# Performance work log

Measured on AMD Instinct MI355X. Metric: run time of the kernel, lower is better.

Reference implementation:

```python
import jax, jax.numpy as jnp
import numpy as np

B, T = 512, 64
C_IN, C_HID, C_OUT = 512, 512, 256
SIZE_INP = C_IN + C_HID + C_OUT  # 1280
SIZE_GATES = 4 * C_HID           # 2048


def setup_inputs() -> dict:
    key = jax.random.key(0)
    k1, k2, k3, k4, k5 = jax.random.split(key, 5)
    s_rnn = 1.0 / np.sqrt(SIZE_INP)
    s_feat = 1.0 / np.sqrt(C_HID)
    return {
        "z": jax.random.normal(k1, (B, T, C_IN, 1, 1), dtype=jnp.float32),
        "r0": jnp.zeros((B, C_OUT, 1, 1), dtype=jnp.float32),
        "h0": jnp.zeros((B, C_HID, 1, 1), dtype=jnp.float32),
        "c0": jnp.zeros((B, C_HID, 1, 1), dtype=jnp.float32),
        "W_rnn": jax.random.uniform(k2, (SIZE_GATES, SIZE_INP), jnp.float32, -s_rnn, s_rnn),
        "b_rnn": jax.random.uniform(k3, (SIZE_GATES,), jnp.float32, -s_rnn, s_rnn),
        "W_feat": jax.random.uniform(k4, (C_OUT, C_HID), jnp.float32, -s_feat, s_feat),
        "b_feat": jax.random.uniform(k5, (C_OUT,), jnp.float32, -s_feat, s_feat),
    }


def reference(z, r0, h0, c0, W_rnn, b_rnn, W_feat, b_feat):
    # 1x1 convs on [B,C,1,1] tensors are plain matmuls over channels.
    zs = z[..., 0, 0]  # [B, T, C_in]

    def step(carry, z_t):
        r, h, c = carry  # [B,Cout], [B,H], [B,H]
        inp = jnp.concatenate([r, h, z_t], axis=1)          # [B, 1280]
        gates = inp @ W_rnn.T + b_rnn                       # [B, 4H]
        f, i, s, o = jnp.split(gates, 4, axis=1)            # torch.chunk order
        c_n = jax.nn.sigmoid(f) * c + jax.nn.sigmoid(i) * jnp.tanh(s)
        h_n = jax.nn.sigmoid(o) * jnp.tanh(c_n)
        r_n = r + h_n @ W_feat.T + b_feat
        return (r_n, h_n, c_n), None

    carry0 = (r0[..., 0, 0], h0[..., 0, 0], c0[..., 0, 0])
    (r, h, c), _ = jax.lax.scan(step, carry0, jnp.swapaxes(zs, 0, 1))
    return r[..., None, None], (h[..., None, None], c[..., None, None])
```

## Files before the change

kernel.cpp:

```cpp
#include <hip/hip_runtime.h>
#include <hip/hip_fp16.h>


using f32x4 = __attribute__((ext_vector_type(4))) float;
using f16x8 = __attribute__((ext_vector_type(8))) _Float16;
using fp16x2 = __attribute__((ext_vector_type(2))) __fp16;

union U4H8 { uint4 u; f16x8 h; fp16x2 p[4]; };

__device__ __forceinline__ float sigm(float x){ return 1.0f/(1.0f + __expf(-x)); }
__device__ __forceinline__ float tanhfast(float x){
  x = fminf(fmaxf(x, -30.f), 30.f);
  float e = __expf(2.0f*x);
  return (e - 1.0f)/(e + 1.0f);
}

#define MFMA16(a,b,c) __builtin_amdgcn_mfma_f32_16x16x32_f16((a).h,(b).h,(c),0,0,0)


__global__ void k_wft(const float* __restrict__ wf, float* __restrict__ wft){
  int idx = blockIdx.x*256 + threadIdx.x;
  int c = idx & 511; int j = idx >> 9;
  wft[c*256 + j] = wf[idx];
}

__global__ void k_bias2(const float* __restrict__ wrnn, const float* __restrict__ brnn,
                        const float* __restrict__ bfeat, float* __restrict__ biasp){
  int wv = (blockIdx.x*256 + threadIdx.x) >> 6;
  int lane = threadIdx.x & 63;
  int g = (wv&3)*512 + (wv>>2);
  const float* wr = wrnn + (size_t)g*1280;
  float s = 0.f;
  for (int j = lane; j < 256; j += 64) s += bfeat[j]*wr[j];
  for (int off = 32; off; off >>= 1) s += __shfl_down(s, off, 64);
  if (lane == 0) biasp[wv] = brnn[g] + s;
}

__global__ void k_whp4(const float* __restrict__ wrnn, const float* __restrict__ wft,
                       float* __restrict__ whp_part){
  int s = blockIdx.x >> 8;
  int tl = blockIdx.x & 255;
  int bn = tl & 31, bk = tl >> 5;
  __shared__ float wrs[64][37];
  __shared__ float wfs[64][37];
  int tid = threadIdx.x;
  int tn = tid & 15, tk = tid >> 4;
  float accv[4][4];
  #pragma unroll
  for (int x=0;x<4;x++) for (int y=0;y<4;y++) accv[x][y]=0.f;
  for (int jc = s*64; jc < s*64+64; jc += 32){
    __syncthreads();
    for (int idx = tid; idx < 64*32; idx += 256){
      int r = idx >> 5, j = idx & 31;
      int n = bn*64 + r; int g = (n&3)*512 + (n>>2);
      wrs[r][j] = wrnn[(size_t)g*1280 + jc + j];
      wfs[r][j] = wft[(bk*64 + r)*256 + jc + j];
    }
    __syncthreads();
    for (int j=0;j<32;j++){
      float a[4], b[4];
      #pragma unroll
      for (int x=0;x<4;x++){ a[x] = wfs[tk*4+x][j]; b[x] = wrs[tn*4+x][j]; }
      #pragma unroll
      for (int x=0;x<4;x++)
        #pragma unroll
        for (int y=0;y<4;y++) accv[x][y] += a[x]*b[y];
    }
  }
  float* dst = whp_part + (size_t)s*1048576;
  for (int x=0;x<4;x++){
    int kk = bk*64 + tk*4 + x;
    for (int y=0;y<4;y++){
      int n = bn*64 + tn*4 + y;
      dst[(size_t)kk*2048 + n] = accv[x][y];
    }
  }
}

__global__ void k_whpadd(const float* __restrict__ p, float* __restrict__ o){
  int i = (blockIdx.x*256 + threadIdx.x)*4;
  float4 a = *(const float4*)(p + i);
  float4 b = *(const float4*)(p + 1048576 + i);
  float4 c = *(const float4*)(p + 2097152 + i);
  float4 d = *(const float4*)(p + 3145728 + i);
  float4 r;
  r.x = a.x+b.x+c.x+d.x; r.y = a.y+b.y+c.y+d.y;
  r.z = a.z+b.z+c.z+d.z; r.w = a.w+b.w+c.w+d.w;
  *(float4*)(o + i) = r;
}

__global__ void k_rinit(const float* __restrict__ r0, const float* __restrict__ h0,
                        const float* __restrict__ wft, const float* __restrict__ bfeat,
                        float* __restrict__ rd32, __half* __restrict__ rd16){
  __shared__ float hs[512];
  int row = blockIdx.x; int j = threadIdx.x;
  for (int k = threadIdx.x; k < 512; k += 256) hs[k] = h0[row*512 + k];
  __syncthreads();
  float acc = 0.f;
  for (int k=0;k<512;k++) acc += hs[k]*wft[k*256 + j];
  float rr = r0[row*256 + j] - acc - bfeat[j];
  rd32[row*256 + j] = rr;
  int ridx = (((row>>4)*8 + (j>>5))*64 + (row&15) + (((j&31)>>3)<<4))*8 + (j&7);
  rd16[ridx] = __float2half(rr);
}

__global__ void k_packh0(const float* __restrict__ h0, const float* __restrict__ c0,
                         __half* __restrict__ h16, float* __restrict__ c32){
  int idx = blockIdx.x*256 + threadIdx.x;
  int e = idx & 7, l = (idx>>3) & 63, kc = (idx>>9) & 15, mt = idx >> 13;
  int row = mt*16 + (l&15);
  int k = kc*32 + ((l>>4)<<3) + e;
  h16[idx] = __float2half(h0[row*512 + k]);
  c32[idx] = c0[idx];
}

__global__ void k_pack(const float* __restrict__ wrnn, const float* __restrict__ whp32,
                       const float* __restrict__ wfeat, __half* __restrict__ dst,
                       int mode, int NT16, int KCH){
  int tot = NT16*KCH*512;
  for (int idx = blockIdx.x*256 + threadIdx.x; idx < tot; idx += gridDim.x*256){
    int e = idx & 7; int l = (idx>>3) & 63;
    int kc = (idx>>9) % KCH; int nt = (idx>>9) / KCH;
    int k = kc*32 + ((l>>4)<<3) + e;
    int n = nt*16 + (l&15);
    float v;
    if (mode == 0){
      int g = (n&3)*512 + (n>>2);
      if (k < 256) v = wrnn[(size_t)g*1280 + k];
      else         v = whp32[(size_t)(k-256)*2048 + n] + wrnn[(size_t)g*1280 + k];
    } else if (mode == 2){
      int g = (n&3)*512 + (n>>2);
      v = wrnn[(size_t)g*1280 + 768 + k];
    } else {
      v = wfeat[(size_t)n*512 + k];
    }
    dst[idx] = __float2half(v);
  }
}

__global__ void k_zpackall(const float* __restrict__ z, __half* __restrict__ z16){
  int u = blockIdx.x*256 + threadIdx.x;
  int k0 = (u & 63) * 8;
  int b4 = (u >> 6) & 127;
  int t  = u >> 13;
  int b = b4 * 4;
  int frag = (t*32 + (b>>4))*16 + (k0>>5);
  uint4 wv[4];
  #pragma unroll
  for (int j=0;j<4;j++){
    const float4* src = (const float4*)(z + ((size_t)((b+j)*64 + t))*512 + k0);
    float4 f0 = src[0], f1 = src[1];
    U4H8 a;
    a.p[0] = __builtin_amdgcn_cvt_pkrtz(f0.x, f0.y);
    a.p[1] = __builtin_amdgcn_cvt_pkrtz(f0.z, f0.w);
    a.p[2] = __builtin_amdgcn_cvt_pkrtz(f1.x, f1.y);
    a.p[3] = __builtin_amdgcn_cvt_pkrtz(f1.z, f1.w);
    wv[j] = a.u;
  }
  uint4* dst = (uint4*)z16 + (size_t)frag*64 + (b & 15) + (((k0 & 31) >> 3) << 4);
  #pragma unroll
  for (int j=0;j<4;j++) dst[j] = wv[j];
}

__global__ __launch_bounds__(512) void k_gzbig(const __half* __restrict__ z16,
    const __half* __restrict__ bpz, const float* __restrict__ biasp,
    __half* __restrict__ gz){
  const int tid = threadIdx.x, lane = tid & 63, w = tid >> 6;
  const int wr = w >> 2, wc = w & 3;
  const int xcd = blockIdx.x & 7;
  const int bn  = (blockIdx.x >> 3) & 15;
  const int bmh = blockIdx.x >> 7;
  const int bm  = xcd*32 + bmh;
  const int tt = bm >> 2, bq = bm & 3;
  const int mt0 = tt*32 + bq*8 + wr*4;
  const int nt0 = bn*8 + wc*2;
  const uint4* A = (const uint4*)z16 + (size_t)(mt0*16)*64 + lane;
  const uint4* B = (const uint4*)bpz + (size_t)(nt0*16)*64 + lane;
  f32x4 acc[4][2];
  #pragma unroll
  for (int mi=0;mi<4;mi++){ acc[mi][0]=(f32x4){0,0,0,0}; acc[mi][1]=(f32x4){0,0,0,0}; }
  #pragma unroll 4
  for (int kc=0; kc<16; ++kc){
    U4H8 b0v, b1v;
    b0v.u = B[kc*64];
    b1v.u = B[(16+kc)*64];
    #pragma unroll
    for (int mi=0; mi<4; mi++){
      U4H8 a;
      a.u = A[(mi*16 + kc)*64];
      acc[mi][0] = MFMA16(a, b0v, acc[mi][0]);
      acc[mi][1] = MFMA16(a, b1v, acc[mi][1]);
    }
  }
  #pragma unroll
  for (int ns=0; ns<2; ns++){
    int n = (nt0 + ns)*16 + (lane & 15);
    float bp = biasp[n];
    #pragma unroll
    for (int mi=0; mi<4; mi++){
      #pragma unroll
      for (int i=0; i<4; i++){
        int brow = bq*128 + wr*64 + mi*16 + ((lane>>4)<<2) + i;
        gz[((size_t)(tt*512 + brow))*2048 + n] = __float2half(acc[mi][ns][i] + bp);
      }
    }
  }
}

__global__ __launch_bounds__(640) void k_stepF(
    const __half* __restrict__ rd16_in, const __half* __restrict__ h16_in,
    float* __restrict__ rd32,
    __half* __restrict__ rd16_out, __half* __restrict__ h16_out,
    float* __restrict__ c32,
    const __half* __restrict__ gz,
    const __half* __restrict__ bp_rec, const __half* __restrict__ bf_pack,
    const float* __restrict__ bfeat,
    float* __restrict__ out_h, float* __restrict__ out_c, float* __restrict__ out_r,
    int step, int mode){
  __shared__ float cls[64][69];
  const int tid = threadIdx.x, lane = tid & 63;
  const int bid = blockIdx.x;
  const int bm = (bid>>3) & 7;
  const int bn = (bid&7)*4 + (bid>>6);

  if (tid < 512){
    if (mode == 0){
      const int w = tid >> 6, wr = w >> 2, wc = w & 3;
      f32x4 a0A=(f32x4){0,0,0,0}, a0B=(f32x4){0,0,0,0};
      f32x4 a1A=(f32x4){0,0,0,0}, a1B=(f32x4){0,0,0,0};
      const int mtA = bm*4 + wr*2;
      const int nt  = bn*4 + wc;
      const uint4* a0p = (const uint4*)rd16_in + (size_t)(mtA*8)*64 + lane;
      const uint4* a1p = a0p + 8*64;
      const uint4* h0p = (const uint4*)h16_in + (size_t)(mtA*16)*64 + lane;
      const uint4* h1p = h0p + 16*64;
      const uint4* bp  = (const uint4*)bp_rec + (size_t)(nt*24)*64 + lane;
      #pragma unroll
      for (int kc=0; kc<4; ++kc){
        U4H8 a0,a1,b;
        a0.u = a0p[kc*64]; a1.u = a1p[kc*64]; b.u = bp[kc*64];
        a0A = MFMA16(a0,b,a0A);
        a1A = MFMA16(a1,b,a1A);
      }
      #pragma unroll
      for (int kc=4; kc<8; ++kc){
        U4H8 a0,a1,b;
        a0.u = a0p[kc*64]; a1.u = a1p[kc*64]; b.u = bp[kc*64];
        a0B = MFMA16(a0,b,a0B);
        a1B = MFMA16(a1,b,a1B);
      }
      #pragma unroll 4
      for (int kc=0; kc<8; ++kc){
        U4H8 a0,a1,b;
        a0.u = h0p[kc*64]; a1.u = h1p[kc*64]; b.u = bp[(8+kc)*64];
        a0A = MFMA16(a0,b,a0A);
        a1A = MFMA16(a1,b,a1A);
      }
      #pragma unroll 4
      for (int kc=8; kc<16; ++kc){
        U4H8 a0,a1,b;
        a0.u = h0p[kc*64]; a1.u = h1p[kc*64]; b.u = bp[(8+kc)*64];
        a0B = MFMA16(a0,b,a0B);
        a1B = MFMA16(a1,b,a1B);
      }
      const f32x4 acc0 = a0A + a0B;
      const f32x4 acc1 = a1A + a1B;
      #pragma unroll
      for (int i=0; i<4; i++){
        cls[wr*32 +      ((lane>>4)<<2) + i][wc*16 + (lane&15)] = acc0[i];
        cls[wr*32 + 16 + ((lane>>4)<<2) + i][wc*16 + (lane&15)] = acc1[i];
      }
    }
  } else {
    const int w2 = (tid - 512) >> 6;
    const int rb = bid*2 + w2;
    const int mt = rb >> 4;
    const int nc = rb & 15;
    const uint4* hp = (const uint4*)h16_in + (size_t)(mt*16)*64 + lane;
    const uint4* bf = (const uint4*)bf_pack + (size_t)(nc*16)*64 + lane;
    f32x4 r0v = (f32x4){0,0,0,0}, r1v = (f32x4){0,0,0,0};
    #pragma unroll 4
    for (int kc=0; kc<8; ++kc){
      U4H8 a,b;
      a.u = hp[kc*64]; b.u = bf[kc*64];
      r0v = MFMA16(a,b,r0v);
    }
    #pragma unroll 4
    for (int kc=8; kc<16; ++kc){
      U4H8 a,b;
      a.u = hp[kc*64]; b.u = bf[kc*64];
      r1v = MFMA16(a,b,r1v);
    }
    const f32x4 racc = r0v + r1v;
    const int col = nc*16 + (lane&15);
    const float bfv = bfeat[col];
    #pragma unroll
    for (int i=0;i<4;i++){
      const int grow = mt*16 + ((lane>>4)<<2) + i;
      const size_t x = (size_t)grow*256 + col;
      const float rr = racc[i] + rd32[x] + bfv;
      if (mode == 1){
        out_r[x] = rr;
      } else {
        rd32[x] = rr;
        const int ridx = (((grow>>4)*8 + (col>>5))*64
                          + (grow&15) + (((col&31)>>3)<<4))*8 + (col&7);
        rd16_out[ridx] = __float2half(rr);
      }
    }
  }

  if (mode == 0){
    __syncthreads();
    if (tid < 512){
      const __half* gzt = gz + (size_t)step*1048576;
      #pragma unroll
      for (int rep=0; rep<2; rep++){
        int idx = rep*512 + tid;
        int jl = idx & 15, row = idx >> 4;
        int grow = bm*64 + row;
        int j = bn*16 + jl;
        const __half2* gp = (const __half2*)(gzt + (size_t)grow*2048 + bn*64 + jl*4);
        __half2 p0 = gp[0], p1 = gp[1];
        float g0 = cls[row][jl*4+0] + __half2float(p0.x);
        float g1 = cls[row][jl*4+1] + __half2float(p0.y);
        float g2 = cls[row][jl*4+2] + __half2float(p1.x);
        float g3 = cls[row][jl*4+3] + __half2float(p1.y);
        float cold = c32[(size_t)grow*512 + j];
        float f  = sigm(g0);
        float ii = sigm(g1);
        float s  = tanhfast(g2);
        float o  = sigm(g3);
        float cn = f*cold + ii*s;
        float hn = o*tanhfast(cn);
        c32[(size_t)grow*512 + j] = cn;
        int hidx = (((grow>>4)*16 + (j>>5))*64 + (grow&15) + (((j&31)>>3)<<4))*8 + (j&7);
        h16_out[hidx] = __float2half(hn);
        if (step == 63){
          out_h[(size_t)grow*512 + j] = hn;
          out_c[(size_t)grow*512 + j] = cn;
        }
      }
    }
  }
}

extern "C" void kernel_launch(void* const* d_in, const int* in_sizes, int n_in,
                              void* d_out, int out_size, void* d_ws, size_t ws_size,
                              hipStream_t stream){
  const float* z     = (const float*)d_in[0];
  const float* r0    = (const float*)d_in[1];
  const float* h0    = (const float*)d_in[2];
  const float* c0    = (const float*)d_in[3];
  const float* wrnn  = (const float*)d_in[4];
  const float* brnn  = (const float*)d_in[5];
  const float* wfeat = (const float*)d_in[6];
  const float* bfeat = (const float*)d_in[7];
  float* out = (float*)d_out;

  char* wsb = (char*)d_ws;
  size_t off = 0;
  auto alloc = [&](size_t bytes)->char*{
    char* p = wsb + off; off = (off + bytes + 255) & ~(size_t)255; return p;
  };
  __half* z16     = (__half*)alloc((size_t)64*512*512*2);
  __half* bp_rec  = (__half*)alloc((size_t)128*24*512*2);
  __half* bpz     = (__half*)alloc((size_t)128*16*512*2);
  __half* bf_pack = (__half*)alloc((size_t)16*16*512*2);
  float*  biasp   = (float*) alloc(2048*4);
  float*  wft32   = (float*) alloc((size_t)512*256*4);
  __half* h16A    = (__half*)alloc((size_t)512*512*2);
  __half* h16B    = (__half*)alloc((size_t)512*512*2);
  __half* rd16A   = (__half*)alloc((size_t)512*256*2);
  __half* rd16B   = (__half*)alloc((size_t)512*256*2);
  float*  rd32    = (float*) alloc((size_t)512*256*4);
  float*  c32     = (float*) alloc((size_t)512*512*4);
  __half* gz      = (__half*)alloc((size_t)64*512*2048*2);
  (void)ws_size;
  float* whp32    = (float*)gz;
  float* whp_part = (float*)gz + 1048576;

  k_wft     <<<dim3(512),  dim3(256), 0, stream>>>(wfeat, wft32);
  k_bias2   <<<dim3(512),  dim3(256), 0, stream>>>(wrnn, brnn, bfeat, biasp);
  k_whp4    <<<dim3(1024), dim3(256), 0, stream>>>(wrnn, wft32, whp_part);
  k_whpadd  <<<dim3(1024), dim3(256), 0, stream>>>(whp_part, whp32);
  k_rinit   <<<dim3(512),  dim3(256), 0, stream>>>(r0, h0, wft32, bfeat, rd32, rd16A);
  k_packh0  <<<dim3(1024), dim3(256), 0, stream>>>(h0, c0, h16A, c32);
  k_pack    <<<dim3(1024), dim3(256), 0, stream>>>(wrnn, whp32, wfeat, bp_rec, 0, 128, 24);
  k_pack    <<<dim3(1024), dim3(256), 0, stream>>>(wrnn, whp32, wfeat, bpz,    2, 128, 16);
  k_pack    <<<dim3(64),   dim3(256), 0, stream>>>(wrnn, whp32, wfeat, bf_pack,3,  16, 16);
  k_zpackall<<<dim3(2048), dim3(256), 0, stream>>>(z, z16);
  k_gzbig   <<<dim3(4096), dim3(512), 0, stream>>>(z16, bpz, biasp, gz);

  __half* h16in = h16A;  __half* h16out = h16B;
  __half* rd16in = rd16A; __half* rd16out = rd16B;
  for (int t = 1; t <= 64; ++t){
    k_stepF<<<dim3(256), dim3(640), 0, stream>>>(
        rd16in, h16in, rd32, rd16out, h16out, c32, gz,
        bp_rec, bf_pack, bfeat,
        out + 131072, out + 393216, (float*)nullptr, t-1, 0);
    __half* th;
    th = h16in; h16in = h16out; h16out = th;
    th = rd16in; rd16in = rd16out; rd16out = th;
  }
  k_stepF<<<dim3(256), dim3(640), 0, stream>>>(
      rd16in, h16in, rd32, rd16out, h16out, c32, gz,
      bp_rec, bf_pack, bfeat,
      (float*)nullptr, (float*)nullptr, out, 64, 1);
}
```

Before: 808.7 us.

## Merge preprocessing kernels and prefetch gate/state loads in recurrent step

Folds the many setup kernels (weight transpose, bias, partial-sum reduction, packing, z conversion) into two multi-role launches, so fewer launches are issued and the whp partial sums are reduced inline during packing. Inside the per-step kernel, the precomputed z-gate values and old cell state are loaded before the MFMA loop, and the r-update warps load rd32 early, to hide global latency. The r-update branch now runs in parallel with the gate branch instead of before a shared barrier. The gz GEMM unroll drops from 4 to 2. The merged kernels use heterogeneous block roles, and the early loads raise register pressure.

Measured after the change: 752.1 us, median of 2. 7.0% less time.

```diff
diff --git a/kernel.cpp b/kernel.cpp
--- a/kernel.cpp
+++ b/kernel.cpp
@@ -7,6 +7,7 @@
 using fp16x2 = __attribute__((ext_vector_type(2))) __fp16;
 
 union U4H8 { uint4 u; f16x8 h; fp16x2 p[4]; };
+union GZU { uint2 u; __half2 h2[2]; };
 
 __device__ __forceinline__ float sigm(float x){ return 1.0f/(1.0f + __expf(-x)); }
 __device__ __forceinline__ float tanhfast(float x){
@@ -17,23 +18,24 @@
 
 #define MFMA16(a,b,c) __builtin_amdgcn_mfma_f32_16x16x32_f16((a).h,(b).h,(c),0,0,0)
 
-
-__global__ void k_wft(const float* __restrict__ wf, float* __restrict__ wft){
-  int idx = blockIdx.x*256 + threadIdx.x;
-  int c = idx & 511; int j = idx >> 9;
-  wft[c*256 + j] = wf[idx];
-}
-
-__global__ void k_bias2(const float* __restrict__ wrnn, const float* __restrict__ brnn,
-                        const float* __restrict__ bfeat, float* __restrict__ biasp){
-  int wv = (blockIdx.x*256 + threadIdx.x) >> 6;
-  int lane = threadIdx.x & 63;
-  int g = (wv&3)*512 + (wv>>2);
-  const float* wr = wrnn + (size_t)g*1280;
-  float s = 0.f;
-  for (int j = lane; j < 256; j += 64) s += bfeat[j]*wr[j];
-  for (int off = 32; off; off >>= 1) s += __shfl_down(s, off, 64);
-  if (lane == 0) biasp[wv] = brnn[g] + s;
+__global__ void k_init(const float* __restrict__ wfeat, const float* __restrict__ wrnn,
+                       const float* __restrict__ brnn, const float* __restrict__ bfeat,
+                       float* __restrict__ wft, float* __restrict__ biasp){
+  const int bid = blockIdx.x, tid = threadIdx.x;
+  if (bid < 512){
+    int idx = bid*256 + tid;
+    int c = idx & 511; int j = idx >> 9;
+    wft[c*256 + j] = wfeat[idx];
+  } else {
+    int wv = ((bid-512)*256 + tid) >> 6;
+    int lane = tid & 63;
+    int g = (wv&3)*512 + (wv>>2);
+    const float* wr = wrnn + (size_t)g*1280;
+    float s = 0.f;
+    for (int j = lane; j < 256; j += 64) s += bfeat[j]*wr[j];
+    for (int off = 32; off; off >>= 1) s += __shfl_down(s, off, 64);
+    if (lane == 0) biasp[wv] = brnn[g] + s;
+  }
 }
 
 __global__ void k_whp4(const float* __restrict__ wrnn, const float* __restrict__ wft,
@@ -77,89 +79,94 @@
   }
 }
 
-__global__ void k_whpadd(const float* __restrict__ p, float* __restrict__ o){
-  int i = (blockIdx.x*256 + threadIdx.x)*4;
-  float4 a = *(const float4*)(p + i);
-  float4 b = *(const float4*)(p + 1048576 + i);
-  float4 c = *(const float4*)(p + 2097152 + i);
-  float4 d = *(const float4*)(p + 3145728 + i);
-  float4 r;
-  r.x = a.x+b.x+c.x+d.x; r.y = a.y+b.y+c.y+d.y;
-  r.z = a.z+b.z+c.z+d.z; r.w = a.w+b.w+c.w+d.w;
-  *(float4*)(o + i) = r;
-}
-
-__global__ void k_rinit(const float* __restrict__ r0, const float* __restrict__ h0,
-                        const float* __restrict__ wft, const float* __restrict__ bfeat,
-                        float* __restrict__ rd32, __half* __restrict__ rd16){
+__global__ void k_prep(const float* __restrict__ z,
+                       const float* __restrict__ r0, const float* __restrict__ h0,
+                       const float* __restrict__ c0,
+                       const float* __restrict__ wrnn, const float* __restrict__ wfeat,
+                       const float* __restrict__ wft, const float* __restrict__ bfeat,
+                       const float* __restrict__ whp_part,
+                       float* __restrict__ rd32, __half* __restrict__ rd16,
+                       __half* __restrict__ h16, float* __restrict__ c32,
+                       __half* __restrict__ bp_rec, __half* __restrict__ bpz,
+                       __half* __restrict__ bf_pack, __half* __restrict__ z16){
   __shared__ float hs[512];
-  int row = blockIdx.x; int j = threadIdx.x;
-  for (int k = threadIdx.x; k < 512; k += 256) hs[k] = h0[row*512 + k];
-  __syncthreads();
-  float acc = 0.f;
-  for (int k=0;k<512;k++) acc += hs[k]*wft[k*256 + j];
-  float rr = r0[row*256 + j] - acc - bfeat[j];
-  rd32[row*256 + j] = rr;
-  int ridx = (((row>>4)*8 + (j>>5))*64 + (row&15) + (((j&31)>>3)<<4))*8 + (j&7);
-  rd16[ridx] = __float2half(rr);
-}
-
-__global__ void k_packh0(const float* __restrict__ h0, const float* __restrict__ c0,
-                         __half* __restrict__ h16, float* __restrict__ c32){
-  int idx = blockIdx.x*256 + threadIdx.x;
-  int e = idx & 7, l = (idx>>3) & 63, kc = (idx>>9) & 15, mt = idx >> 13;
-  int row = mt*16 + (l&15);
-  int k = kc*32 + ((l>>4)<<3) + e;
-  h16[idx] = __float2half(h0[row*512 + k]);
-  c32[idx] = c0[idx];
-}
-
-__global__ void k_pack(const float* __restrict__ wrnn, const float* __restrict__ whp32,
-                       const float* __restrict__ wfeat, __half* __restrict__ dst,
-                       int mode, int NT16, int KCH){
-  int tot = NT16*KCH*512;
-  for (int idx = blockIdx.x*256 + threadIdx.x; idx < tot; idx += gridDim.x*256){
-    int e = idx & 7; int l = (idx>>3) & 63;
-    int kc = (idx>>9) % KCH; int nt = (idx>>9) / KCH;
+  const int bid = blockIdx.x, tid = threadIdx.x;
+  if (bid < 512){
+    const int row = bid, j = tid;
+    for (int k = tid; k < 512; k += 256) hs[k] = h0[row*512 + k];
+    __syncthreads();
+    float acc = 0.f;
+    for (int k=0;k<512;k++) acc += hs[k]*wft[k*256 + j];
+    float rr = r0[row*256 + j] - acc - bfeat[j];
+    rd32[row*256 + j] = rr;
+    int ridx = (((row>>4)*8 + (j>>5))*64 + (row&15) + (((j&31)>>3)<<4))*8 + (j&7);
+    rd16[ridx] = __float2half(rr);
+  } else if (bid < 1536){
+    int idx = (bid-512)*256 + tid;
+    int e = idx & 7, l = (idx>>3) & 63, kc = (idx>>9) & 15, mt = idx >> 13;
+    int row = mt*16 + (l&15);
     int k = kc*32 + ((l>>4)<<3) + e;
-    int n = nt*16 + (l&15);
-    float v;
-    if (mode == 0){
+    h16[idx] = __float2half(h0[row*512 + k]);
+    c32[idx] = c0[idx];
+  } else if (bid < 2560){
+    const int tot = 128*24*512;
+    for (int idx = (bid-1536)*256 + tid; idx < tot; idx += 1024*256){
+      int e = idx & 7; int l = (idx>>3) & 63;
+      int kc = (idx>>9) % 24; int nt = (idx>>9) / 24;
+      int k = kc*32 + ((l>>4)<<3) + e;
+      int n = nt*16 + (l&15);
       int g = (n&3)*512 + (n>>2);
+      float v;
       if (k < 256) v = wrnn[(size_t)g*1280 + k];
-      else         v = whp32[(size_t)(k-256)*2048 + n] + wrnn[(size_t)g*1280 + k];
-    } else if (mode == 2){
+      else {
+        size_t o = (size_t)(k-256)*2048 + n;
+        v = whp_part[o] + whp_part[1048576+o] + whp_part[2097152+o]
+            + whp_part[3145728+o] + wrnn[(size_t)g*1280 + k];
+      }
+      bp_rec[idx] = __float2half(v);
+    }
+  } else if (bid < 3072){
+    const int tot = 128*16*512;
+    for (int idx = (bid-2560)*256 + tid; idx < tot; idx += 512*256){
+      int e = idx & 7; int l = (idx>>3) & 63;
+      int kc = (idx>>9) & 15; int nt = (idx>>9) >> 4;
+      int k = kc*32 + ((l>>4)<<3) + e;
+      int n = nt*16 + (l&15);
       int g = (n&3)*512 + (n>>2);
-      v = wrnn[(size_t)g*1280 + 768 + k];
-    } else {
-      v = wfeat[(size_t)n*512 + k];
-    }
-    dst[idx] = __float2half(v);
-  }
-}
-
-__global__ void k_zpackall(const float* __restrict__ z, __half* __restrict__ z16){
-  int u = blockIdx.x*256 + threadIdx.x;
-  int k0 = (u & 63) * 8;
-  int b4 = (u >> 6) & 127;
-  int t  = u >> 13;
-  int b = b4 * 4;
-  int frag = (t*32 + (b>>4))*16 + (k0>>5);
-  uint4 wv[4];
-  #pragma unroll
-  for (int j=0;j<4;j++){
-    const float4* src = (const float4*)(z + ((size_t)((b+j)*64 + t))*512 + k0);
-    float4 f0 = src[0], f1 = src[1];
-    U4H8 a;
-    a.p[0] = __builtin_amdgcn_cvt_pkrtz(f0.x, f0.y);
-    a.p[1] = __builtin_amdgcn_cvt_pkrtz(f0.z, f0.w);
-    a.p[2] = __builtin_amdgcn_cvt_pkrtz(f1.x, f1.y);
-    a.p[3] = __builtin_amdgcn_cvt_pkrtz(f1.z, f1.w);
-    wv[j] = a.u;
-  }
-  uint4* dst = (uint4*)z16 + (size_t)frag*64 + (b & 15) + (((k0 & 31) >> 3) << 4);
-  #pragma unroll
-  for (int j=0;j<4;j++) dst[j] = wv[j];
+      bpz[idx] = __float2half(wrnn[(size_t)g*1280 + 768 + k]);
+    }
+  } else if (bid < 3136){
+    const int tot = 16*16*512;
+    for (int idx = (bid-3072)*256 + tid; idx < tot; idx += 64*256){
+      int e = idx & 7; int l = (idx>>3) & 63;
+      int kc = (idx>>9) & 15; int nt = (idx>>9) >> 4;
+      int k = kc*32 + ((l>>4)<<3) + e;
+      int n = nt*16 + (l&15);
+      bf_pack[idx] = __float2half(wfeat[(size_t)n*512 + k]);
+    }
+  } else {
+    int u = (bid-3136)*256 + tid;
+    int k0 = (u & 63) * 8;
+    int b4 = (u >> 6) & 127;
+    int t  = u >> 13;
+    int b = b4 * 4;
+    int frag = (t*32 + (b>>4))*16 + (k0>>5);
+    uint4 wv[4];
+    #pragma unroll
+    for (int j=0;j<4;j++){
+      const float4* src = (const float4*)(z + ((size_t)((b+j)*64 + t))*512 + k0);
+      float4 f0 = src[0], f1 = src[1];
+      U4H8 a;
+      a.p[0] = __builtin_amdgcn_cvt_pkrtz(f0.x, f0.y);
+      a.p[1] = __builtin_amdgcn_cvt_pkrtz(f0.z, f0.w);
+      a.p[2] = __builtin_amdgcn_cvt_pkrtz(f1.x, f1.y);
+      a.p[3] = __builtin_amdgcn_cvt_pkrtz(f1.z, f1.w);
+      wv[j] = a.u;
+    }
+    uint4* dst = (uint4*)z16 + (size_t)frag*64 + (b & 15) + (((k0 & 31) >> 3) << 4);
+    #pragma unroll
+    for (int j=0;j<4;j++) dst[j] = wv[j];
+  }
 }
 
 __global__ __launch_bounds__(512) void k_gzbig(const __half* __restrict__ z16,
@@ -179,7 +186,7 @@
   f32x4 acc[4][2];
   #pragma unroll
   for (int mi=0;mi<4;mi++){ acc[mi][0]=(f32x4){0,0,0,0}; acc[mi][1]=(f32x4){0,0,0,0}; }
-  #pragma unroll 4
+  #pragma unroll 2
   for (int kc=0; kc<16; ++kc){
     U4H8 b0v, b1v;
     b0v.u = B[kc*64];
@@ -225,6 +232,17 @@
 
   if (tid < 512){
     if (mode == 0){
+      const __half* gzt = gz + (size_t)step*1048576;
+      const int jl0 = tid & 15,        row0 = tid >> 4;
+      const int jl1 = (512+tid) & 15,  row1 = (512+tid) >> 4;
+      const int gr0 = bm*64 + row0, j0 = bn*16 + jl0;
+      const int gr1 = bm*64 + row1, j1 = bn*16 + jl1;
+      GZU gu0, gu1;
+      gu0.u = *(const uint2*)(gzt + (size_t)gr0*2048 + bn*64 + jl0*4);
+      gu1.u = *(const uint2*)(gzt + (size_t)gr1*2048 + bn*64 + jl1*4);
+      const float cold0 = c32[(size_t)gr0*512 + j0];
+      const float cold1 = c32[(size_t)gr1*512 + j1];
+
       const int w = tid >> 6, wr = w >> 2, wc = w & 3;
       f32x4 a0A=(f32x4){0,0,0,0}, a0B=(f32x4){0,0,0,0};
       f32x4 a1A=(f32x4){0,0,0,0}, a1B=(f32x4){0,0,0,0};
@@ -270,63 +288,19 @@
         cls[wr*32 +      ((lane>>4)<<2) + i][wc*16 + (lane&15)] = acc0[i];
         cls[wr*32 + 16 + ((lane>>4)<<2) + i][wc*16 + (lane&15)] = acc1[i];
       }
-    }
-  } else {
-    const int w2 = (tid - 512) >> 6;
-    const int rb = bid*2 + w2;
-    const int mt = rb >> 4;
-    const int nc = rb & 15;
-    const uint4* hp = (const uint4*)h16_in + (size_t)(mt*16)*64 + lane;
-    const uint4* bf = (const uint4*)bf_pack + (size_t)(nc*16)*64 + lane;
-    f32x4 r0v = (f32x4){0,0,0,0}, r1v = (f32x4){0,0,0,0};
-    #pragma unroll 4
-    for (int kc=0; kc<8; ++kc){
-      U4H8 a,b;
-      a.u = hp[kc*64]; b.u = bf[kc*64];
-      r0v = MFMA16(a,b,r0v);
-    }
-    #pragma unroll 4
-    for (int kc=8; kc<16; ++kc){
-      U4H8 a,b;
-      a.u = hp[kc*64]; b.u = bf[kc*64];
-      r1v = MFMA16(a,b,r1v);
-    }
-    const f32x4 racc = r0v + r1v;
-    const int col = nc*16 + (lane&15);
-    const float bfv = bfeat[col];
-    #pragma unroll
-    for (int i=0;i<4;i++){
-      const int grow = mt*16 + ((lane>>4)<<2) + i;
-      const size_t x = (size_t)grow*256 + col;
-      const float rr = racc[i] + rd32[x] + bfv;
-      if (mode == 1){
-        out_r[x] = rr;
-      } else {
-        rd32[x] = rr;
-        const int ridx = (((grow>>4)*8 + (col>>5))*64
-                          + (grow&15) + (((col&31)>>3)<<4))*8 + (col&7);
-        rd16_out[ridx] = __float2half(rr);
-      }
-    }
-  }
-
-  if (mode == 0){
-    __syncthreads();
-    if (tid < 512){
-      const __half* gzt = gz + (size_t)step*1048576;
+      __syncthreads();
       #pragma unroll
       for (int rep=0; rep<2; rep++){
-        int idx = rep*512 + tid;
-        int jl = idx & 15, row = idx >> 4;
-        int grow = bm*64 + row;
-        int j = bn*16 + jl;
-        const __half2* gp = (const __half2*)(gzt + (size_t)grow*2048 + bn*64 + jl*4);
-        __half2 p0 = gp[0], p1 = gp[1];
-        float g0 = cls[row][jl*4+0] + __half2float(p0.x);
-        float g1 = cls[row][jl*4+1] + __half2float(p0.y);
-        float g2 = cls[row][jl*4+2] + __half2float(p1.x);
-        float g3 = cls[row][jl*4+3] + __half2float(p1.y);
-        float cold = c32[(size_t)grow*512 + j];
+        const int row = rep ? row1 : row0;
+        const int jl  = rep ? jl1  : jl0;
+        const int grow = rep ? gr1 : gr0;
+        const int j   = rep ? j1 : j0;
+        const GZU gu  = rep ? gu1 : gu0;
+        const float cold = rep ? cold1 : cold0;
+        float g0 = cls[row][jl*4+0] + __half2float(gu.h2[0].x);
+        float g1 = cls[row][jl*4+1] + __half2float(gu.h2[0].y);
+        float g2 = cls[row][jl*4+2] + __half2float(gu.h2[1].x);
+        float g3 = cls[row][jl*4+3] + __half2float(gu.h2[1].y);
         float f  = sigm(g0);
         float ii = sigm(g1);
         float s  = tanhfast(g2);
@@ -340,6 +314,49 @@
           out_h[(size_t)grow*512 + j] = hn;
           out_c[(size_t)grow*512 + j] = cn;
         }
+      }
+    }
+  } else {
+    const int w2 = (tid - 512) >> 6;
+    const int rb = bid*2 + w2;
+    const int mt = rb >> 4;
+    const int nc = rb & 15;
+    const int col = nc*16 + (lane&15);
+    float rdp[4];
+    #pragma unroll
+    for (int i=0;i<4;i++){
+      const int grow = mt*16 + ((lane>>4)<<2) + i;
+      rdp[i] = rd32[(size_t)grow*256 + col];
+    }
+    const float bfv = bfeat[col];
+    const uint4* hp = (const uint4*)h16_in + (size_t)(mt*16)*64 + lane;
+    const uint4* bf = (const uint4*)bf_pack + (size_t)(nc*16)*64 + lane;
+    f32x4 r0v = (f32x4){0,0,0,0}, r1v = (f32x4){0,0,0,0};
+    #pragma unroll 4
+    for (int kc=0; kc<8; ++kc){
+      U4H8 a,b;
+      a.u = hp[kc*64]; b.u = bf[kc*64];
+      r0v = MFMA16(a,b,r0v);
+    }
+    #pragma unroll 4
+    for (int kc=8; kc<16; ++kc){
+      U4H8 a,b;
+      a.u = hp[kc*64]; b.u = bf[kc*64];
+      r1v = MFMA16(a,b,r1v);
+    }
+    const f32x4 racc = r0v + r1v;
+    #pragma unroll
+    for (int i=0;i<4;i++){
+      const int grow = mt*16 + ((lane>>4)<<2) + i;
+      const size_t x = (size_t)grow*256 + col;
+      const float rr = racc[i] + rdp[i] + bfv;
+      if (mode == 1){
+        out_r[x] = rr;
+      } else {
+        rd32[x] = rr;
+        const int ridx = (((grow>>4)*8 + (col>>5))*64
+                          + (grow&15) + (((col&31)>>3)<<4))*8 + (col&7);
+        rd16_out[ridx] = __float2half(rr);
       }
     }
   }
@@ -377,20 +394,14 @@
   float*  c32     = (float*) alloc((size_t)512*512*4);
   __half* gz      = (__half*)alloc((size_t)64*512*2048*2);
   (void)ws_size;
-  float* whp32    = (float*)gz;
   float* whp_part = (float*)gz + 1048576;
 
-  k_wft     <<<dim3(512),  dim3(256), 0, stream>>>(wfeat, wft32);
-  k_bias2   <<<dim3(512),  dim3(256), 0, stream>>>(wrnn, brnn, bfeat, biasp);
-  k_whp4    <<<dim3(1024), dim3(256), 0, stream>>>(wrnn, wft32, whp_part);
-  k_whpadd  <<<dim3(1024), dim3(256), 0, stream>>>(whp_part, whp32);
-  k_rinit   <<<dim3(512),  dim3(256), 0, stream>>>(r0, h0, wft32, bfeat, rd32, rd16A);
-  k_packh0  <<<dim3(1024), dim3(256), 0, stream>>>(h0, c0, h16A, c32);
-  k_pack    <<<dim3(1024), dim3(256), 0, stream>>>(wrnn, whp32, wfeat, bp_rec, 0, 128, 24);
-  k_pack    <<<dim3(1024), dim3(256), 0, stream>>>(wrnn, whp32, wfeat, bpz,    2, 128, 16);
-  k_pack    <<<dim3(64),   dim3(256), 0, stream>>>(wrnn, whp32, wfeat, bf_pack,3,  16, 16);
-  k_zpackall<<<dim3(2048), dim3(256), 0, stream>>>(z, z16);
-  k_gzbig   <<<dim3(4096), dim3(512), 0, stream>>>(z16, bpz, biasp, gz);
+  k_init <<<dim3(1024), dim3(256), 0, stream>>>(wfeat, wrnn, brnn, bfeat, wft32, biasp);
+  k_whp4 <<<dim3(1024), dim3(256), 0, stream>>>(wrnn, wft32, whp_part);
+  k_prep <<<dim3(5184), dim3(256), 0, stream>>>(z, r0, h0, c0, wrnn, wfeat, wft32,
+                                                bfeat, whp_part, rd32, rd16A, h16A,
+                                                c32, bp_rec, bpz, bf_pack, z16);
+  k_gzbig<<<dim3(4096), dim3(512), 0, stream>>>(z16, bpz, biasp, gz);
 
   __half* h16in = h16A;  __half* h16out = h16B;
   __half* rd16in = rd16A; __half* rd16out = rd16B;
```
